# Optimization experiments

Measured on AMD Instinct MI355X. Metric: run time of the kernel, lower is better.

## Reference

```python
import jax, jax.numpy as jnp
import numpy as np

BS, L, D, K, G, E = 512, 128, 512, 30, 8, 2048
H = E // 2  # MLP hidden = embed_dim // 2


def setup_inputs():
    key = jax.random.key(0)
    ks = jax.random.split(key, 8)
    features = jax.random.normal(ks[0], (BS, L, D), jnp.float32)
    atten = jax.random.uniform(ks[1], (BS, L, L), jnp.float32)
    rng = np.random.default_rng(0)
    lens = rng.integers(34, L - 1, size=BS)          # caption lengths (>= 34 so lengths-2 > K)
    toks = rng.integers(1, 1000, size=(BS, L))
    pos = np.arange(L)[None, :]
    text = np.where(pos < lens[:, None], toks, 0)    # zero padding
    text[np.arange(BS), lens - 1] = 49407            # eos = max token id -> argmax finds it
    text = jnp.asarray(text, jnp.int32)
    pid = jnp.asarray(np.repeat(np.arange(BS // G), G), jnp.int32)  # 64 groups of size G=8
    dlp_w = jax.random.normal(ks[2], (G, D), jnp.float32)           # weights['weight_8']
    dlp_b = jnp.zeros((G,), jnp.float32)                            # biases['bias_8']
    dlp_lw = jax.random.normal(ks[3], (K * G, E), jnp.float32) * 0.05  # linears['linear_8']
    dlp_lb = jnp.zeros((E,), jnp.float32)
    mlp_w1 = jax.random.normal(ks[4], (D, H), jnp.float32) * 0.04
    mlp_b1 = jnp.zeros((H,), jnp.float32)
    bn_g = jnp.ones((H,), jnp.float32)
    bn_b = jnp.zeros((H,), jnp.float32)
    mlp_w2 = jax.random.normal(ks[5], (H, E), jnp.float32) * 0.03
    mlp_b2 = jnp.zeros((E,), jnp.float32)
    return dict(features=features, atten=atten, text=text, pid=pid,
                dlp_w=dlp_w, dlp_b=dlp_b, dlp_lw=dlp_lw, dlp_lb=dlp_lb,
                mlp_w1=mlp_w1, mlp_b1=mlp_b1, bn_g=bn_g, bn_b=bn_b,
                mlp_w2=mlp_w2, mlp_b2=mlp_b2)


def _l2norm(x, eps=1e-8):
    return x / (jnp.sqrt(jnp.sum(x * x, axis=-1, keepdims=True)) + eps)


def _groups_from_pid(pid_np):
    # replicates the pid_dist==0 grouping + dedup-by-member-set, preserving first-seen order
    groups, order = {}, []
    for i, p in enumerate(pid_np.tolist()):
        if p not in groups:
            groups[p] = []
            order.append(p)
        groups[p].append(i)
    return [groups[p] for p in order]


def reference(features, atten, text, pid, dlp_w, dlp_b, dlp_lw, dlp_lb,
              mlp_w1, mlp_b1, bn_g, bn_b, mlp_w2, mlp_b2):
    bs = features.shape[0]
    b = jnp.arange(bs)
    mask = (text != 0).astype(features.dtype)                  # [bs, L]
    lengths = mask.sum(1) - 2.0                                # [bs]
    eos = jnp.argmax(text, axis=-1)                            # [bs]
    att = atten.at[b, :, eos].set(-1.0).at[:, :, 0].set(-1.0)
    row = att[b, eos, :] * mask                                # [bs, L]
    idx = jax.lax.top_k(row, K)[1]                             # [bs, K] topk token indices
    feats = jnp.take_along_axis(features, idx[:, :, None], axis=1)  # [bs, K, D]

    # pid-based dynamic grouping (host-side; pid is an index input, static)
    glists = _groups_from_pid(np.asarray(pid))
    assert {len(g) for g in glists} == {G}, 'expert params provided for group size G only'
    gi = np.asarray(glists)                                    # [ng, G]
    xg = feats[gi].reshape(gi.shape[0], G * K, D)              # concat group members: [ng, G*K, D]
    # F.linear(x, W[G,D], b).T  ->  [ng, G, G*K]
    h = jnp.einsum('ntd,gd->ngt', xg, dlp_w) + dlp_b[None, :, None]
    yg = h @ dlp_lw + dlp_lb                                   # linear_G: [ng, G, E]
    # scatter-combine each member's row back to its batch position
    new_base = jnp.zeros((bs, E), feats.dtype).at[gi.reshape(-1)].set(yg.reshape(-1, E))
    new_base = _l2norm(new_base)

    # MLP (Linear -> BatchNorm1d(train stats) -> ReLU -> Linear) on l2-normed gathered feats
    x = _l2norm(feats).reshape(bs * K, D) @ mlp_w1 + mlp_b1
    mu, var = x.mean(0), x.var(0)
    x = jax.nn.relu((x - mu) / jnp.sqrt(var + 1e-5) * bn_g + bn_b)
    x = (x @ mlp_w2 + mlp_b2).reshape(bs, K, E)

    # maxk_pool1d_var with pool k=1: per-channel max over first min(length, K) rows
    lens = jnp.minimum(lengths, K).astype(jnp.int32)
    valid = jnp.arange(K)[None, :] < lens[:, None]             # [bs, K]
    pooled = jnp.max(jnp.where(valid[:, :, None], x, -jnp.inf), axis=1)  # [bs, E]
    return (pooled + new_base).astype(jnp.float32)
```

## Files before the change

kernel.cpp:

```cpp
#include <hip/hip_runtime.h>
#include <hip/hip_bf16.h>

#define BS 512
#define LL 128
#define DD 512
#define KK 30
#define GG 8
#define EE 2048
#define HH 1024
#define NROWS (BS*KK)
#define NG (BS/GG)

typedef __attribute__((ext_vector_type(8))) short bf16x8;
typedef __attribute__((ext_vector_type(4))) float f32x4;
typedef __attribute__((address_space(1))) const unsigned int gu32;
typedef __attribute__((address_space(3))) unsigned int lu32;

__device__ __forceinline__ unsigned short f2bf(float f){
  unsigned int x = __float_as_uint(f);
  x = (x + 0x7FFFu + ((x >> 16) & 1u)) >> 16;
  return (unsigned short)x;
}
__device__ __forceinline__ float bf2f(unsigned short u){
  return __uint_as_float(((unsigned int)u) << 16);
}
__device__ __forceinline__ unsigned fkey(float f){
  unsigned b = __float_as_uint(f);
  return (b & 0x80000000u) ? ~b : (b | 0x80000000u);
}
__device__ __forceinline__ float fdec(unsigned k){
  unsigned b = (k & 0x80000000u) ? (k & 0x7FFFFFFFu) : ~k;
  return __uint_as_float(b);
}

#define FENCE asm volatile("" ::: "memory")
#define BARR  do{ FENCE; __builtin_amdgcn_s_barrier(); FENCE; }while(0)
#define VMW(n) asm volatile("s_waitcnt vmcnt(" #n ")" ::: "memory")

__global__ __launch_bounds__(256) void k_pg(const float* __restrict__ atten,
                                            const int* __restrict__ text,
                                            const float* __restrict__ features,
                                            const float* __restrict__ dlp_w,
                                            const float* __restrict__ dlp_b,
                                            const float* __restrict__ w1,
                                            unsigned short* __restrict__ w1t,
                                            unsigned short* __restrict__ nfeats,
                                            float* __restrict__ hval,
                                            int* __restrict__ lensk){
  __shared__ int sidx[KK];
  __shared__ float tile[32][33];

  if(blockIdx.x >= BS){
    const int blk = blockIdx.x - BS;
    const int n0 = (blk & 31)*32, k0 = (blk >> 5)*32;
    const int r = threadIdx.x >> 3, c4 = (threadIdx.x & 7)*4;
    const float4 v = *(const float4*)(w1 + (size_t)(k0 + r)*HH + n0 + c4);
    tile[r][c4+0] = v.x; tile[r][c4+1] = v.y; tile[r][c4+2] = v.z; tile[r][c4+3] = v.w;
    __syncthreads();
    ushort4 u;
    u.x = f2bf(tile[c4+0][r]); u.y = f2bf(tile[c4+1][r]);
    u.z = f2bf(tile[c4+2][r]); u.w = f2bf(tile[c4+3][r]);
    *(ushort4*)(w1t + (size_t)(n0 + r)*DD + k0 + c4) = u;
    return;
  }

  const int b = blockIdx.x;
  const int tid = threadIdx.x;
  const int wv = tid >> 6, lane = tid & 63;

  if(wv == 0){
    const int t0 = text[b*LL + lane];
    const int t1 = text[b*LL + 64 + lane];
    int v, vi;
    if(t1 > t0){ v = t1; vi = lane + 64; } else { v = t0; vi = lane; }
#pragma unroll
    for(int off = 32; off; off >>= 1){
      const int ov = __shfl_xor(v, off), oi = __shfl_xor(vi, off);
      if(ov > v || (ov == v && oi < vi)){ v = ov; vi = oi; }
    }
    const int eos = vi;
    const unsigned long long mb0 = __ballot(t0 != 0), mb1 = __ballot(t1 != 0);
    if(lane == 0) lensk[b] = min(__popcll(mb0) + __popcll(mb1) - 2, KK);

    const float a0 = atten[(size_t)b*LL*LL + (size_t)eos*LL + lane];
    const float a1 = atten[(size_t)b*LL*LL + (size_t)eos*LL + 64 + lane];
    float r0 = (t0 == 0) ? 0.f : ((lane == 0 || lane == eos) ? -1.f : a0);
    float r1 = (t1 == 0) ? 0.f : ((lane + 64 == eos) ? -1.f : a1);
    for(int k = 0; k < KK; k++){
      float mv; int mi;
      if(r1 > r0){ mv = r1; mi = lane + 64; } else { mv = r0; mi = lane; }
#pragma unroll
      for(int off = 32; off; off >>= 1){
        const float ov = __shfl_xor(mv, off); const int oi = __shfl_xor(mi, off);
        if(ov > mv || (ov == mv && oi < mi)){ mv = ov; mi = oi; }
      }
      if(lane == 0) sidx[k] = mi;
      if(mi == lane)      r0 = -3.f;
      if(mi == lane + 64) r1 = -3.f;
    }
  }
  __syncthreads();

  for(int it = 0; it < 8; it++){
    const int r = it*4 + wv;
    if(r >= KK) break;
    const int l = sidx[r];
    const float4* fp = (const float4*)features + ((size_t)b*LL + l)*(DD/4);
    const float4 v0 = fp[lane], v1 = fp[64 + lane];
    float ss = v0.x*v0.x + v0.y*v0.y + v0.z*v0.z + v0.w*v0.w
             + v1.x*v1.x + v1.y*v1.y + v1.z*v1.z + v1.w*v1.w;
#pragma unroll
    for(int off = 32; off; off >>= 1) ss += __shfl_xor(ss, off);
    float hout = 0.f;
#pragma unroll
    for(int g = 0; g < GG; g++){
      const float4 w0 = ((const float4*)dlp_w)[g*(DD/4) + lane];
      const float4 w1v = ((const float4*)dlp_w)[g*(DD/4) + 64 + lane];
      float hg = v0.x*w0.x + v0.y*w0.y + v0.z*w0.z + v0.w*w0.w
               + v1.x*w1v.x + v1.y*w1v.y + v1.z*w1v.z + v1.w*w1v.w;
#pragma unroll
      for(int off = 32; off; off >>= 1) hg += __shfl_xor(hg, off);
      if(lane == g) hout = hg;
    }
    if(lane < GG) hval[(size_t)(b*KK + r)*GG + lane] = hout + dlp_b[lane];
    const float rn = 1.0f / (sqrtf(ss) + 1e-8f);
    ushort4 u0, u1;
    u0.x = f2bf(v0.x*rn); u0.y = f2bf(v0.y*rn); u0.z = f2bf(v0.z*rn); u0.w = f2bf(v0.w*rn);
    u1.x = f2bf(v1.x*rn); u1.y = f2bf(v1.y*rn); u1.z = f2bf(v1.z*rn); u1.w = f2bf(v1.w*rn);
    ushort4* np = (ushort4*)nfeats + (size_t)(b*KK + r)*(DD/4);
    np[lane] = u0; np[64 + lane] = u1;
  }
}

__global__ __launch_bounds__(256) void k_dlp(const float* __restrict__ hval,
                                             const float* __restrict__ dlp_lw,
                                             const float* __restrict__ dlp_lb,
                                             unsigned short* __restrict__ nbbf){
  const int et = blockIdx.x;
  const int n  = blockIdx.y;
  const int tid = threadIdx.x;
  __shared__ float hs[GG][GG*KK];
  for(int i = tid; i < GG*GG*KK; i += 256){
    const int g = i / (GG*KK), tt = i % (GG*KK);
    const int m = tt / KK, kq = tt % KK;
    hs[g][tt] = hval[(size_t)(((n*GG + m)*KK) + kq)*GG + g];
  }
  __syncthreads();
  const int h = tid >> 7, c = tid & 127;
  const int e = et*128 + c;
  float acc[4] = {0.f, 0.f, 0.f, 0.f};
#pragma unroll 4
  for(int k = 0; k < GG*KK; k++){
    const float w = dlp_lw[(size_t)k*EE + e];
#pragma unroll
    for(int rr = 0; rr < 4; rr++) acc[rr] += hs[h*4 + rr][k] * w;
  }
  const float lb = dlp_lb[e];
#pragma unroll
  for(int rr = 0; rr < 4; rr++)
    nbbf[(size_t)(n*GG + h*4 + rr)*EE + e] = f2bf(acc[rr] + lb);
}

__global__ __launch_bounds__(256) void k_l2nb(unsigned short* __restrict__ nbbf){
  const int b = blockIdx.x, t = threadIdx.x;
  uint4* p = (uint4*)(nbbf + (size_t)b*EE);
  uint4 u = p[t];
  unsigned short* us = (unsigned short*)&u;
  float f[8]; float ss = 0.f;
#pragma unroll
  for(int j = 0; j < 8; j++){ f[j] = bf2f(us[j]); ss += f[j]*f[j]; }
#pragma unroll
  for(int off = 32; off > 0; off >>= 1) ss += __shfl_down(ss, off);
  __shared__ float red[4];
  __shared__ float s_rn;
  if((t & 63) == 0) red[t >> 6] = ss;
  __syncthreads();
  if(t == 0) s_rn = 1.0f / (sqrtf(red[0] + red[1] + red[2] + red[3]) + 1e-8f);
  __syncthreads();
  const float rn = s_rn;
#pragma unroll
  for(int j = 0; j < 8; j++) us[j] = f2bf(f[j]*rn);
  p[t] = u;
}

__global__ __launch_bounds__(256, 2) void k_g1(const unsigned short* __restrict__ A,
                                               const unsigned short* __restrict__ Bt,
                                               const float* __restrict__ bias,
                                               unsigned short* __restrict__ obf,
                                               float* __restrict__ psum,
                                               float* __restrict__ psq){
  const int KD = DD, ND = HH, NBX = HH/128;
  __shared__ short S[2][2][128*64];
  const int tid  = threadIdx.x;
  const int wave = tid >> 6, lane = tid & 63;
  const int wr = wave >> 1, wc = wave & 1;
  const int lrow = lane & 15, kg = lane >> 4;

  const int nwg = gridDim.x, cpx = nwg >> 3;
  const int bid = (blockIdx.x & 7)*cpx + (blockIdx.x >> 3);
  const int bx = bid % NBX, by = bid / NBX;
  const int m0 = by*128, n0 = bx*128;

  const unsigned short* Ab = A  + (size_t)m0*KD;
  const unsigned short* Bb = Bt + (size_t)n0*KD;

#define G1STG(tt, p) { \
  _Pragma("unroll") \
  for(int c = 0; c < 4; c++){ \
    const int i_ = tid + c*256; const int r_ = i_ >> 3; \
    const int g_ = (i_ & 7) ^ (r_ & 7); \
    __builtin_amdgcn_global_load_lds((gu32*)(Ab + (size_t)r_*KD + (tt)*64 + g_*8), \
                                     (lu32*)(&S[p][0][i_*8]), 16, 0, 0); \
  } \
  _Pragma("unroll") \
  for(int c = 0; c < 4; c++){ \
    const int i_ = tid + c*256; const int r_ = i_ >> 3; \
    const int g_ = (i_ & 7) ^ (r_ & 7); \
    __builtin_amdgcn_global_load_lds((gu32*)(Bb + (size_t)r_*KD + (tt)*64 + g_*8), \
                                     (lu32*)(&S[p][1][i_*8]), 16, 0, 0); \
  } \
}

  f32x4 acc[4][4] = {};
  const int NT = KD/64;
  G1STG(0, 0)
  G1STG(1, 1)

  const int arow = wr*64 + lrow;
  const int brow = wc*64 + lrow;
  const int gx0 = (kg       ^ (lrow & 7))*8;
  const int gx1 = ((4 + kg) ^ (lrow & 7))*8;

#pragma unroll 1
  for(int t = 0; t < NT; t++){
    const int p = t & 1;
    if(t < NT-1) VMW(8);
    else         VMW(0);
    BARR;
    const short* Abuf = &S[p][0][0];
    const short* Bbuf = &S[p][1][0];
    bf16x8 af[4], bg[4];
#pragma unroll
    for(int n = 0; n < 4; n++) bg[n] = *(const bf16x8*)(Bbuf + (brow + n*16)*64 + gx0);
#pragma unroll
    for(int m = 0; m < 4; m++) af[m] = *(const bf16x8*)(Abuf + (arow + m*16)*64 + gx0);
    __builtin_amdgcn_s_setprio(1);
#pragma unroll
    for(int m = 0; m < 4; m++)
#pragma unroll
      for(int n = 0; n < 4; n++)
        acc[m][n] = __builtin_amdgcn_mfma_f32_16x16x32_bf16(af[m], bg[n], acc[m][n], 0, 0, 0);
    __builtin_amdgcn_s_setprio(0);
#pragma unroll
    for(int n = 0; n < 4; n++) bg[n] = *(const bf16x8*)(Bbuf + (brow + n*16)*64 + gx1);
#pragma unroll
    for(int m = 0; m < 4; m++) af[m] = *(const bf16x8*)(Abuf + (arow + m*16)*64 + gx1);
    __builtin_amdgcn_s_setprio(1);
#pragma unroll
    for(int m = 0; m < 4; m++)
#pragma unroll
      for(int n = 0; n < 4; n++)
        acc[m][n] = __builtin_amdgcn_mfma_f32_16x16x32_bf16(af[m], bg[n], acc[m][n], 0, 0, 0);
    __builtin_amdgcn_s_setprio(0);
    BARR;
    if(t + 2 < NT){ G1STG(t+2, p) }
  }
#undef G1STG

  const int colb = n0 + wc*64 + lrow;
#pragma unroll
  for(int n = 0; n < 4; n++){
    const float bb = bias[colb + n*16];
    float sv = 0.f, qv = 0.f;
#pragma unroll
    for(int m = 0; m < 4; m++)
#pragma unroll
      for(int r = 0; r < 4; r++){
        const float v = acc[m][n][r] + bb; sv += v; qv += v*v;
      }
    sv += __shfl_xor(sv, 16); sv += __shfl_xor(sv, 32);
    qv += __shfl_xor(qv, 16); qv += __shfl_xor(qv, 32);
    if(lane < 16){
      psum[(size_t)(by*2 + wr)*ND + colb + n*16] = sv;
      psq [(size_t)(by*2 + wr)*ND + colb + n*16] = qv;
    }
#pragma unroll
    for(int m = 0; m < 4; m++){
      const int row = m0 + wr*64 + m*16 + kg*4;
#pragma unroll
      for(int r = 0; r < 4; r++)
        obf[(size_t)(row + r)*ND + colb + n*16] = f2bf(acc[m][n][r] + bb);
    }
  }
}

__global__ __launch_bounds__(256) void k_bnw(const float* __restrict__ psum,
                                             const float* __restrict__ psq,
                                             const float* __restrict__ bn_g,
                                             const float* __restrict__ bn_b,
                                             float* __restrict__ sc,
                                             float* __restrict__ sh,
                                             const float* __restrict__ w2,
                                             unsigned short* __restrict__ w2t){
  if(blockIdx.x < 4){
    const int c = blockIdx.x*256 + threadIdx.x;
    float s = 0.f, q = 0.f;
    for(int i = 0; i < 240; i++){ s += psum[(size_t)i*HH + c]; q += psq[(size_t)i*HH + c]; }
    const float mu  = s * (1.0f/NROWS);
    const float var = q * (1.0f/NROWS) - mu*mu;
    const float sv  = bn_g[c] / sqrtf(var + 1e-5f);
    sc[c] = sv;
    sh[c] = bn_b[c] - mu*sv;
    return;
  }
  __shared__ float tile[32][33];
  const int blk = blockIdx.x - 4;
  const int n0 = (blk & 63)*32, k0 = (blk >> 6)*32;
  const int r = threadIdx.x >> 3, c4 = (threadIdx.x & 7)*4;
  const float4 v = *(const float4*)(w2 + (size_t)(k0 + r)*EE + n0 + c4);
  tile[r][c4+0] = v.x; tile[r][c4+1] = v.y; tile[r][c4+2] = v.z; tile[r][c4+3] = v.w;
  __syncthreads();
  ushort4 u;
  u.x = f2bf(tile[c4+0][r]); u.y = f2bf(tile[c4+1][r]);
  u.z = f2bf(tile[c4+2][r]); u.w = f2bf(tile[c4+3][r]);
  *(ushort4*)(w2t + (size_t)(n0 + r)*HH + k0 + c4) = u;
}

__global__ __launch_bounds__(256) void k_bnrelu(unsigned short* __restrict__ x1,
                                                const float* __restrict__ sc,
                                                const float* __restrict__ sh,
                                                unsigned* __restrict__ pkey){
  const size_t i = (size_t)blockIdx.x*256 + threadIdx.x;
  const int c0 = (int)((i*8) & (HH-1));
  uint4 u = ((uint4*)x1)[i];
  unsigned short* us = (unsigned short*)&u;
  const float4 s0 = *(const float4*)(sc + c0), s1 = *(const float4*)(sc + c0 + 4);
  const float4 h0 = *(const float4*)(sh + c0), h1 = *(const float4*)(sh + c0 + 4);
  const float scv[8] = {s0.x,s0.y,s0.z,s0.w,s1.x,s1.y,s1.z,s1.w};
  const float shv[8] = {h0.x,h0.y,h0.z,h0.w,h1.x,h1.y,h1.z,h1.w};
#pragma unroll
  for(int j = 0; j < 8; j++)
    us[j] = f2bf(fmaxf(bf2f(us[j])*scv[j] + shv[j], 0.f));
  ((uint4*)x1)[i] = u;
  if(blockIdx.x < 1024)
    ((uint4*)pkey)[blockIdx.x*256 + threadIdx.x] =
        make_uint4(0x007FFFFFu, 0x007FFFFFu, 0x007FFFFFu, 0x007FFFFFu);
}

__global__ __launch_bounds__(256, 2) void k_g2(const unsigned short* __restrict__ A,
                                               const unsigned short* __restrict__ Bt,
                                               const int* __restrict__ lensk,
                                               unsigned* __restrict__ pkey){
  const int KD = HH, ND = EE, NBX = EE/128;
  __shared__ short S[2][2][128*64];
  const int tid  = threadIdx.x;
  const int wave = tid >> 6, lane = tid & 63;
  const int wr = wave >> 1, wc = wave & 1;
  const int lrow = lane & 15, kg = lane >> 4;

  const int nwg = gridDim.x, cpx = nwg >> 3;
  const int bid = (blockIdx.x & 7)*cpx + (blockIdx.x >> 3);
  const int bx = bid % NBX, by = bid / NBX;
  const int m0 = by*128, n0 = bx*128;

  const unsigned short* Ab = A  + (size_t)m0*KD;
  const unsigned short* Bb = Bt + (size_t)n0*KD;

#define G2STG(tt, p) { \
  _Pragma("unroll") \
  for(int c = 0; c < 4; c++){ \
    const int i_ = tid + c*256; const int r_ = i_ >> 3; \
    const int g_ = (i_ & 7) ^ (r_ & 7); \
    __builtin_amdgcn_global_load_lds((gu32*)(Ab + (size_t)r_*KD + (tt)*64 + g_*8), \
                                     (lu32*)(&S[p][0][i_*8]), 16, 0, 0); \
  } \
  _Pragma("unroll") \
  for(int c = 0; c < 4; c++){ \
    const int i_ = tid + c*256; const int r_ = i_ >> 3; \
    const int g_ = (i_ & 7) ^ (r_ & 7); \
    __builtin_amdgcn_global_load_lds((gu32*)(Bb + (size_t)r_*KD + (tt)*64 + g_*8), \
                                     (lu32*)(&S[p][1][i_*8]), 16, 0, 0); \
  } \
}

  f32x4 acc[4][4] = {};
  const int NT = KD/64;
  G2STG(0, 0)
  G2STG(1, 1)

  const int arow = wr*64 + lrow;
  const int brow = wc*64 + lrow;
  const int gx0 = (kg       ^ (lrow & 7))*8;
  const int gx1 = ((4 + kg) ^ (lrow & 7))*8;

#pragma unroll 1
  for(int t = 0; t < NT; t++){
    const int p = t & 1;
    if(t < NT-1) VMW(8);
    else         VMW(0);
    BARR;
    const short* Abuf = &S[p][0][0];
    const short* Bbuf = &S[p][1][0];
    bf16x8 af[4], bg[4];
#pragma unroll
    for(int n = 0; n < 4; n++) bg[n] = *(const bf16x8*)(Bbuf + (brow + n*16)*64 + gx0);
#pragma unroll
    for(int m = 0; m < 4; m++) af[m] = *(const bf16x8*)(Abuf + (arow + m*16)*64 + gx0);
    __builtin_amdgcn_s_setprio(1);
#pragma unroll
    for(int m = 0; m < 4; m++)
#pragma unroll
      for(int n = 0; n < 4; n++)
        acc[m][n] = __builtin_amdgcn_mfma_f32_16x16x32_bf16(af[m], bg[n], acc[m][n], 0, 0, 0);
    __builtin_amdgcn_s_setprio(0);
#pragma unroll
    for(int n = 0; n < 4; n++) bg[n] = *(const bf16x8*)(Bbuf + (brow + n*16)*64 + gx1);
#pragma unroll
    for(int m = 0; m < 4; m++) af[m] = *(const bf16x8*)(Abuf + (arow + m*16)*64 + gx1);
    __builtin_amdgcn_s_setprio(1);
#pragma unroll
    for(int m = 0; m < 4; m++)
#pragma unroll
      for(int n = 0; n < 4; n++)
        acc[m][n] = __builtin_amdgcn_mfma_f32_16x16x32_bf16(af[m], bg[n], acc[m][n], 0, 0, 0);
    __builtin_amdgcn_s_setprio(0);
    BARR;
    if(t + 2 < NT){ G2STG(t+2, p) }
  }
#undef G2STG

  __syncthreads();
  unsigned* pool = (unsigned*)&S[0][0][0];
  const int b0 = m0 / KK;
  const int b1 = (m0 + 127) / KK;
  const int nseg = b1 - b0 + 1;
  for(int i = tid; i < nseg*128; i += 256) pool[i] = 0x007FFFFFu;
  __syncthreads();
  const int lcol = wc*64 + lrow;
  {
    int cur_b = -1;
    float mx[4];
#pragma unroll
    for(int m = 0; m < 4; m++){
#pragma unroll
      for(int r = 0; r < 4; r++){
        const int row = m0 + wr*64 + m*16 + kg*4 + r;
        const int bt = row / KK;
        const int rr = row - bt*KK;
        if(bt != cur_b){
          if(cur_b >= 0){
#pragma unroll
            for(int n = 0; n < 4; n++)
              atomicMax(&pool[(cur_b - b0)*128 + lcol + n*16], fkey(mx[n]));
          }
          cur_b = bt;
#pragma unroll
          for(int n = 0; n < 4; n++) mx[n] = -INFINITY;
        }
        if(rr < lensk[bt]){
#pragma unroll
          for(int n = 0; n < 4; n++) mx[n] = fmaxf(mx[n], acc[m][n][r]);
        }
      }
    }
#pragma unroll
    for(int n = 0; n < 4; n++)
      atomicMax(&pool[(cur_b - b0)*128 + lcol + n*16], fkey(mx[n]));
  }
  __syncthreads();
  for(int e = tid; e < nseg*128; e += 256){
    const int seg = e >> 7, col = e & 127;
    atomicMax(&pkey[(size_t)(b0 + seg)*ND + n0 + col], pool[e]);
  }
}

__global__ __launch_bounds__(256) void k_final(const unsigned* __restrict__ pkey,
                                               const float* __restrict__ b2,
                                               const unsigned short* __restrict__ nbbf,
                                               float* __restrict__ out){
  const size_t i = (size_t)blockIdx.x*256 + threadIdx.x;
  const int c0 = (int)((i*4) & (EE-1));
  const uint4 k = ((const uint4*)pkey)[i];
  const ushort4 nb4 = ((const ushort4*)nbbf)[i];
  const float4 b = *(const float4*)(b2 + c0);
  float4 o;
  o.x = fdec(k.x) + b.x + bf2f(nb4.x);
  o.y = fdec(k.y) + b.y + bf2f(nb4.y);
  o.z = fdec(k.z) + b.z + bf2f(nb4.z);
  o.w = fdec(k.w) + b.w + bf2f(nb4.w);
  ((float4*)out)[i] = o;
}

extern "C" void kernel_launch(void* const* d_in, const int* in_sizes, int n_in,
                              void* d_out, int out_size, void* d_ws, size_t ws_size,
                              hipStream_t stream){
  const float* features = (const float*)d_in[0];
  const float* atten    = (const float*)d_in[1];
  const int*   text     = (const int*)  d_in[2];
  const float* dlp_w    = (const float*)d_in[4];
  const float* dlp_b    = (const float*)d_in[5];
  const float* dlp_lw   = (const float*)d_in[6];
  const float* dlp_lb   = (const float*)d_in[7];
  const float* w1       = (const float*)d_in[8];
  const float* b1       = (const float*)d_in[9];
  const float* bn_g     = (const float*)d_in[10];
  const float* bn_b     = (const float*)d_in[11];
  const float* w2       = (const float*)d_in[12];
  const float* b2       = (const float*)d_in[13];
  float* out = (float*)d_out;

  char* ws = (char*)d_ws;
  float*          psum   = (float*)(ws + 0);
  float*          psq    = (float*)(ws + 983040);
  unsigned short* w1t    = (unsigned short*)(ws + 1966080);
  float*          hval   = (float*)(ws + 3014656);
  unsigned*       pkey   = (unsigned*)(ws + 0);
  int*            lensk  = (int*)(ws + 4194304);
  float*          sc     = (float*)(ws + 4196352);
  float*          sh     = (float*)(ws + 4200448);
  unsigned short* nfeats = (unsigned short*)(ws + 4204544);
  unsigned short* w2t    = (unsigned short*)(ws + 4204544);
  unsigned short* x1     = (unsigned short*)(ws + 19933184);
  unsigned short* nbbf   = (unsigned short*)(ws + 51390464);

  k_pg<<<BS + 512, 256, 0, stream>>>(atten, text, features, dlp_w, dlp_b,
                                     w1, w1t, nfeats, hval, lensk);
  k_dlp<<<dim3(16, NG), 256, 0, stream>>>(hval, dlp_lw, dlp_lb, nbbf);
  k_l2nb<<<BS, 256, 0, stream>>>(nbbf);
  k_g1<<<(HH/128)*(NROWS/128), 256, 0, stream>>>(nfeats, w1t, b1, x1, psum, psq);
  k_bnw<<<4 + 2048, 256, 0, stream>>>(psum, psq, bn_g, bn_b, sc, sh, w2, w2t);
  k_bnrelu<<<(NROWS*HH/8)/256, 256, 0, stream>>>(x1, sc, sh, pkey);
  k_g2<<<(EE/128)*(NROWS/128), 256, 0, stream>>>(x1, w2t, lensk, pkey);
  k_final<<<(BS*EE/4)/256, 256, 0, stream>>>(pkey, b2, nbbf, out);
}
```

Baseline: 192.3 us.

## Enlarge GEMM2 tiles to 256x256 with 512 threads and fuse new_base L2 norm into final

```diff
diff --git a/kernel.cpp b/kernel.cpp
--- a/kernel.cpp
+++ b/kernel.cpp
@@ -135,11 +135,13 @@
 __global__ __launch_bounds__(256) void k_dlp(const float* __restrict__ hval,
                                              const float* __restrict__ dlp_lw,
                                              const float* __restrict__ dlp_lb,
-                                             unsigned short* __restrict__ nbbf){
+                                             unsigned short* __restrict__ nbbf,
+                                             float* __restrict__ psq2){
   const int et = blockIdx.x;
   const int n  = blockIdx.y;
   const int tid = threadIdx.x;
   __shared__ float hs[GG][GG*KK];
+  __shared__ float red[4][4];
   for(int i = tid; i < GG*GG*KK; i += 256){
     const int g = i / (GG*KK), tt = i % (GG*KK);
     const int m = tt / KK, kq = tt % KK;
@@ -156,31 +158,27 @@
     for(int rr = 0; rr < 4; rr++) acc[rr] += hs[h*4 + rr][k] * w;
   }
   const float lb = dlp_lb[e];
-#pragma unroll
-  for(int rr = 0; rr < 4; rr++)
-    nbbf[(size_t)(n*GG + h*4 + rr)*EE + e] = f2bf(acc[rr] + lb);
-}
-
-__global__ __launch_bounds__(256) void k_l2nb(unsigned short* __restrict__ nbbf){
-  const int b = blockIdx.x, t = threadIdx.x;
-  uint4* p = (uint4*)(nbbf + (size_t)b*EE);
-  uint4 u = p[t];
-  unsigned short* us = (unsigned short*)&u;
-  float f[8]; float ss = 0.f;
-#pragma unroll
-  for(int j = 0; j < 8; j++){ f[j] = bf2f(us[j]); ss += f[j]*f[j]; }
-#pragma unroll
-  for(int off = 32; off > 0; off >>= 1) ss += __shfl_down(ss, off);
-  __shared__ float red[4];
-  __shared__ float s_rn;
-  if((t & 63) == 0) red[t >> 6] = ss;
-  __syncthreads();
-  if(t == 0) s_rn = 1.0f / (sqrtf(red[0] + red[1] + red[2] + red[3]) + 1e-8f);
-  __syncthreads();
-  const float rn = s_rn;
-#pragma unroll
-  for(int j = 0; j < 8; j++) us[j] = f2bf(f[j]*rn);
-  p[t] = u;
+  float sq[4];
+#pragma unroll
+  for(int rr = 0; rr < 4; rr++){
+    const float v = acc[rr] + lb;
+    nbbf[(size_t)(n*GG + h*4 + rr)*EE + e] = f2bf(v);
+    sq[rr] = v*v;
+  }
+#pragma unroll
+  for(int off = 32; off; off >>= 1)
+#pragma unroll
+    for(int rr = 0; rr < 4; rr++) sq[rr] += __shfl_xor(sq[rr], off);
+  const int wv = tid >> 6, lane = tid & 63;
+  if(lane == 0){
+#pragma unroll
+    for(int rr = 0; rr < 4; rr++) red[wv][rr] = sq[rr];
+  }
+  __syncthreads();
+  if(tid < 8){
+    const int hh = tid >> 2, rr = tid & 3;
+    psq2[(size_t)(n*GG + hh*4 + rr)*16 + et] = red[hh*2][rr] + red[hh*2+1][rr];
+  }
 }
 
 __global__ __launch_bounds__(256, 2) void k_g1(const unsigned short* __restrict__ A,
@@ -347,79 +345,67 @@
         make_uint4(0x007FFFFFu, 0x007FFFFFu, 0x007FFFFFu, 0x007FFFFFu);
 }
 
-__global__ __launch_bounds__(256, 2) void k_g2(const unsigned short* __restrict__ A,
+__global__ __launch_bounds__(512, 2) void k_g2(const unsigned short* __restrict__ A,
                                                const unsigned short* __restrict__ Bt,
                                                const int* __restrict__ lensk,
                                                unsigned* __restrict__ pkey){
-  const int KD = HH, ND = EE, NBX = EE/128;
-  __shared__ short S[2][2][128*64];
+  const int KD = HH, ND = EE, NBX = EE/256;
+  __shared__ short S[2][2][256*32];
   const int tid  = threadIdx.x;
   const int wave = tid >> 6, lane = tid & 63;
-  const int wr = wave >> 1, wc = wave & 1;
+  const int wr = wave >> 2, wc = wave & 3;
   const int lrow = lane & 15, kg = lane >> 4;
 
   const int nwg = gridDim.x, cpx = nwg >> 3;
   const int bid = (blockIdx.x & 7)*cpx + (blockIdx.x >> 3);
   const int bx = bid % NBX, by = bid / NBX;
-  const int m0 = by*128, n0 = bx*128;
+  const int m0 = by*256, n0 = bx*256;
 
   const unsigned short* Ab = A  + (size_t)m0*KD;
   const unsigned short* Bb = Bt + (size_t)n0*KD;
 
 #define G2STG(tt, p) { \
   _Pragma("unroll") \
-  for(int c = 0; c < 4; c++){ \
-    const int i_ = tid + c*256; const int r_ = i_ >> 3; \
-    const int g_ = (i_ & 7) ^ (r_ & 7); \
-    __builtin_amdgcn_global_load_lds((gu32*)(Ab + (size_t)r_*KD + (tt)*64 + g_*8), \
+  for(int c = 0; c < 2; c++){ \
+    const int i_ = tid + c*512; const int r_ = i_ >> 2; \
+    const int g_ = (i_ & 3) ^ ((r_ >> 1) & 3); \
+    __builtin_amdgcn_global_load_lds((gu32*)(Ab + (size_t)r_*KD + (tt)*32 + g_*8), \
                                      (lu32*)(&S[p][0][i_*8]), 16, 0, 0); \
   } \
   _Pragma("unroll") \
-  for(int c = 0; c < 4; c++){ \
-    const int i_ = tid + c*256; const int r_ = i_ >> 3; \
-    const int g_ = (i_ & 7) ^ (r_ & 7); \
-    __builtin_amdgcn_global_load_lds((gu32*)(Bb + (size_t)r_*KD + (tt)*64 + g_*8), \
+  for(int c = 0; c < 2; c++){ \
+    const int i_ = tid + c*512; const int r_ = i_ >> 2; \
+    const int g_ = (i_ & 3) ^ ((r_ >> 1) & 3); \
+    __builtin_amdgcn_global_load_lds((gu32*)(Bb + (size_t)r_*KD + (tt)*32 + g_*8), \
                                      (lu32*)(&S[p][1][i_*8]), 16, 0, 0); \
   } \
 }
 
-  f32x4 acc[4][4] = {};
-  const int NT = KD/64;
+  f32x4 acc[8][4] = {};
+  const int NT = KD/32;
   G2STG(0, 0)
   G2STG(1, 1)
 
-  const int arow = wr*64 + lrow;
-  const int brow = wc*64 + lrow;
-  const int gx0 = (kg       ^ (lrow & 7))*8;
-  const int gx1 = ((4 + kg) ^ (lrow & 7))*8;
+  const int arow = wr*128 + lrow;
+  const int brow = wc*64  + lrow;
+  const int sw = (kg ^ ((lrow >> 1) & 3))*8;
 
 #pragma unroll 1
   for(int t = 0; t < NT; t++){
     const int p = t & 1;
-    if(t < NT-1) VMW(8);
+    if(t < NT-1) VMW(4);
     else         VMW(0);
     BARR;
     const short* Abuf = &S[p][0][0];
     const short* Bbuf = &S[p][1][0];
-    bf16x8 af[4], bg[4];
-#pragma unroll
-    for(int n = 0; n < 4; n++) bg[n] = *(const bf16x8*)(Bbuf + (brow + n*16)*64 + gx0);
-#pragma unroll
-    for(int m = 0; m < 4; m++) af[m] = *(const bf16x8*)(Abuf + (arow + m*16)*64 + gx0);
+    bf16x8 af[8], bg[4];
+#pragma unroll
+    for(int n = 0; n < 4; n++) bg[n] = *(const bf16x8*)(Bbuf + (brow + n*16)*32 + sw);
+#pragma unroll
+    for(int m = 0; m < 8; m++) af[m] = *(const bf16x8*)(Abuf + (arow + m*16)*32 + sw);
     __builtin_amdgcn_s_setprio(1);
 #pragma unroll
-    for(int m = 0; m < 4; m++)
-#pragma unroll
-      for(int n = 0; n < 4; n++)
-        acc[m][n] = __builtin_amdgcn_mfma_f32_16x16x32_bf16(af[m], bg[n], acc[m][n], 0, 0, 0);
-    __builtin_amdgcn_s_setprio(0);
-#pragma unroll
-    for(int n = 0; n < 4; n++) bg[n] = *(const bf16x8*)(Bbuf + (brow + n*16)*64 + gx1);
-#pragma unroll
-    for(int m = 0; m < 4; m++) af[m] = *(const bf16x8*)(Abuf + (arow + m*16)*64 + gx1);
-    __builtin_amdgcn_s_setprio(1);
-#pragma unroll
-    for(int m = 0; m < 4; m++)
+    for(int m = 0; m < 8; m++)
 #pragma unroll
       for(int n = 0; n < 4; n++)
         acc[m][n] = __builtin_amdgcn_mfma_f32_16x16x32_bf16(af[m], bg[n], acc[m][n], 0, 0, 0);
@@ -432,26 +418,26 @@
   __syncthreads();
   unsigned* pool = (unsigned*)&S[0][0][0];
   const int b0 = m0 / KK;
-  const int b1 = (m0 + 127) / KK;
+  const int b1 = (m0 + 255) / KK;
   const int nseg = b1 - b0 + 1;
-  for(int i = tid; i < nseg*128; i += 256) pool[i] = 0x007FFFFFu;
+  for(int i = tid; i < nseg*256; i += 512) pool[i] = 0x007FFFFFu;
   __syncthreads();
   const int lcol = wc*64 + lrow;
   {
     int cur_b = -1;
     float mx[4];
 #pragma unroll
-    for(int m = 0; m < 4; m++){
+    for(int m = 0; m < 8; m++){
 #pragma unroll
       for(int r = 0; r < 4; r++){
-        const int row = m0 + wr*64 + m*16 + kg*4 + r;
+        const int row = m0 + wr*128 + m*16 + kg*4 + r;
         const int bt = row / KK;
         const int rr = row - bt*KK;
         if(bt != cur_b){
           if(cur_b >= 0){
 #pragma unroll
             for(int n = 0; n < 4; n++)
-              atomicMax(&pool[(cur_b - b0)*128 + lcol + n*16], fkey(mx[n]));
+              atomicMax(&pool[(cur_b - b0)*256 + lcol + n*16], fkey(mx[n]));
           }
           cur_b = bt;
 #pragma unroll
@@ -465,11 +451,11 @@
     }
 #pragma unroll
     for(int n = 0; n < 4; n++)
-      atomicMax(&pool[(cur_b - b0)*128 + lcol + n*16], fkey(mx[n]));
-  }
-  __syncthreads();
-  for(int e = tid; e < nseg*128; e += 256){
-    const int seg = e >> 7, col = e & 127;
+      atomicMax(&pool[(cur_b - b0)*256 + lcol + n*16], fkey(mx[n]));
+  }
+  __syncthreads();
+  for(int e = tid; e < nseg*256; e += 512){
+    const int seg = e >> 8, col = e & 255;
     atomicMax(&pkey[(size_t)(b0 + seg)*ND + n0 + col], pool[e]);
   }
 }
@@ -477,17 +463,23 @@
 __global__ __launch_bounds__(256) void k_final(const unsigned* __restrict__ pkey,
                                                const float* __restrict__ b2,
                                                const unsigned short* __restrict__ nbbf,
+                                               const float* __restrict__ psq2,
                                                float* __restrict__ out){
   const size_t i = (size_t)blockIdx.x*256 + threadIdx.x;
   const int c0 = (int)((i*4) & (EE-1));
+  const int b = (int)(blockIdx.x >> 1);
+  float ssq = 0.f;
+#pragma unroll
+  for(int j = 0; j < 16; j++) ssq += psq2[(size_t)b*16 + j];
+  const float rn = 1.0f / (sqrtf(ssq) + 1e-8f);
   const uint4 k = ((const uint4*)pkey)[i];
   const ushort4 nb4 = ((const ushort4*)nbbf)[i];
-  const float4 b = *(const float4*)(b2 + c0);
+  const float4 bb = *(const float4*)(b2 + c0);
   float4 o;
-  o.x = fdec(k.x) + b.x + bf2f(nb4.x);
-  o.y = fdec(k.y) + b.y + bf2f(nb4.y);
-  o.z = fdec(k.z) + b.z + bf2f(nb4.z);
-  o.w = fdec(k.w) + b.w + bf2f(nb4.w);
+  o.x = fdec(k.x) + bb.x + bf2f(nb4.x)*rn;
+  o.y = fdec(k.y) + bb.y + bf2f(nb4.y)*rn;
+  o.z = fdec(k.z) + bb.z + bf2f(nb4.z)*rn;
+  o.w = fdec(k.w) + bb.w + bf2f(nb4.w)*rn;
   ((float4*)out)[i] = o;
 }
 
@@ -518,18 +510,18 @@
   int*            lensk  = (int*)(ws + 4194304);
   float*          sc     = (float*)(ws + 4196352);
   float*          sh     = (float*)(ws + 4200448);
-  unsigned short* nfeats = (unsigned short*)(ws + 4204544);
-  unsigned short* w2t    = (unsigned short*)(ws + 4204544);
-  unsigned short* x1     = (unsigned short*)(ws + 19933184);
-  unsigned short* nbbf   = (unsigned short*)(ws + 51390464);
+  float*          psq2   = (float*)(ws + 4204544);
+  unsigned short* nfeats = (unsigned short*)(ws + 4237312);
+  unsigned short* w2t    = (unsigned short*)(ws + 4237312);
+  unsigned short* x1     = (unsigned short*)(ws + 19965952);
+  unsigned short* nbbf   = (unsigned short*)(ws + 51423232);
 
   k_pg<<<BS + 512, 256, 0, stream>>>(atten, text, features, dlp_w, dlp_b,
                                      w1, w1t, nfeats, hval, lensk);
-  k_dlp<<<dim3(16, NG), 256, 0, stream>>>(hval, dlp_lw, dlp_lb, nbbf);
-  k_l2nb<<<BS, 256, 0, stream>>>(nbbf);
+  k_dlp<<<dim3(16, NG), 256, 0, stream>>>(hval, dlp_lw, dlp_lb, nbbf, psq2);
   k_g1<<<(HH/128)*(NROWS/128), 256, 0, stream>>>(nfeats, w1t, b1, x1, psum, psq);
   k_bnw<<<4 + 2048, 256, 0, stream>>>(psum, psq, bn_g, bn_b, sc, sh, w2, w2t);
   k_bnrelu<<<(NROWS*HH/8)/256, 256, 0, stream>>>(x1, sc, sh, pkey);
-  k_g2<<<(EE/128)*(NROWS/128), 256, 0, stream>>>(x1, w2t, lensk, pkey);
-  k_final<<<(BS*EE/4)/256, 256, 0, stream>>>(pkey, b2, nbbf, out);
-}
+  k_g2<<<(EE/256)*(NROWS/256), 512, 0, stream>>>(x1, w2t, lensk, pkey);
+  k_final<<<(BS*EE/4)/256, 256, 0, stream>>>(pkey, b2, nbbf, psq2, out);
+}
```

After: 188.8 us. No clear change (-1.8%).
